# Kernel optimization log

Hardware: AMD Instinct MI355X
Metric: run time of the kernel (lower is better)

## Reference

```python
import jax, jax.numpy as jnp
import numpy as np

B, T, I, H = 128, 256, 512, 1024


def setup_inputs() -> dict:
    key = jax.random.key(0)
    ks = jax.random.split(key, 16)
    s_in = 1.0 / np.sqrt(I)
    s_h = 1.0 / np.sqrt(H)
    d = {
        "x": jax.random.normal(ks[0], (B, T, I), jnp.float32),
        "x_d": jax.random.normal(ks[1], (B, T, I), jnp.float32),
        "hidden": jnp.zeros((B, H), jnp.float32),
        "cell": jnp.zeros((B, H), jnp.float32),
    }
    for j, n in enumerate(["Wii", "Wif", "Wig", "Wio", "Wid", "Wro"]):
        d[n] = (jax.random.normal(ks[2 + j], (H, I), jnp.float32) * s_in)
    for j, n in enumerate(["Whi", "Whf", "Whg", "Who", "Whd"]):
        d[n] = (jax.random.normal(ks[8 + j], (H, H), jnp.float32) * s_h)
    for n in ["bi", "bf", "bg", "bo", "bd", "Wrb"]:
        d[n] = jnp.zeros((H,), jnp.float32)
    return d


def reference(x, x_d, hidden, cell,
              Wii, Whi, bi, Wif, Whf, bf, Wig, Whg, bg,
              Wio, Who, bo, Wid, Whd, bd, Wro, Wrb):
    # Precompute input-to-hidden contributions for all timesteps: (B,T,H)
    pi = jnp.einsum('bti,hi->bth', x, Wii) + bi
    pf = jnp.einsum('bti,hi->bth', x, Wif) + bf
    pg = jnp.einsum('bti,hi->bth', x, Wig) + bg
    po = jnp.einsum('bti,hi->bth', x, Wio) + bo
    pd = jnp.einsum('bti,hi->bth', x_d, Wid) + bd

    def step(carry, inp):
        h, c = carry
        pi_t, pf_t, pg_t, po_t, pd_t = inp  # each (B,H)
        i_t = jax.nn.sigmoid(pi_t + h @ Whi.T)
        f_t = jax.nn.sigmoid(pf_t + h @ Whf.T)
        g_t = jnp.tanh(pg_t + h @ Whg.T)
        o_t = jax.nn.sigmoid(po_t + h @ Who.T)
        d_t = jax.nn.sigmoid(pd_t + h @ Whd.T)
        c_new = f_t * c + i_t * g_t + d_t
        h_new = o_t * jnp.tanh(c_new)
        return (h_new, c_new), h_new

    xs = tuple(jnp.swapaxes(a, 0, 1) for a in (pi, pf, pg, po, pd))  # (T,B,H)
    (h_last, c_last), hs = jax.lax.scan(step, (hidden, cell), xs)
    hs = jnp.swapaxes(hs, 0, 1)  # (B,T,H)

    # Output projection per timestep (original reuses Who for the readout)
    y = jnp.tanh(jnp.einsum('bti,hi->bth', x, Wro)
                 + jnp.einsum('bth,gh->btg', hs, Who) + Wrb)
    return y, h_last, c_last
```

## Files before the change

### kernel.cpp

```cpp
#include <hip/hip_runtime.h>


using bf16x8 = __attribute__((ext_vector_type(8))) __bf16;
using f32x4  = __attribute__((ext_vector_type(4))) float;

#define MFMA16(a, b, c) __builtin_amdgcn_mfma_f32_16x16x32_bf16(a, b, c, 0, 0, 0)

static __device__ __forceinline__ float b2f(ushort u) {
  union { unsigned int i; float f; } v; v.i = ((unsigned int)u) << 16; return v.f;
}
static __device__ __forceinline__ ushort f2b(float f) {
  union { float f; unsigned int i; } v; v.f = f;
  unsigned int x = v.i;
  return (ushort)((x + 0x7fffu + ((x >> 16) & 1u)) >> 16);
}
static __device__ __forceinline__ float sigm(float x) {
  return 1.0f / (1.0f + __expf(-x));
}
static __device__ __forceinline__ float tanhfast(float x) {
  float e = __expf(2.0f * x);
  return 1.0f - 2.0f / (e + 1.0f);
}

__global__ __launch_bounds__(256) void cvt_kernel(const float* __restrict__ src,
                                                  ushort* __restrict__ dst, int n)
{
  int i = (blockIdx.x * 256 + threadIdx.x) * 4;
  if (i < n) {
    float4 v = *(const float4*)(src + i);
    ushort4 o;
    o.x = f2b(v.x); o.y = f2b(v.y); o.z = f2b(v.z); o.w = f2b(v.w);
    *(ushort4*)(dst + i) = o;
  }
}

static __device__ __forceinline__ void gemm_kloop(
    const ushort* __restrict__ A, int lda,
    const ushort* __restrict__ Bw, int ldb, int K,
    ushort* As, ushort* Bs, f32x4 (&acc)[4][4])
{
  const int tid = threadIdx.x;
  const int l = tid & 63, w = tid >> 6;
  const int wm = (w >> 1) * 64, wn = (w & 1) * 64;
  const int lr = l & 15, quad = l >> 4;
  bf16x8* Asv = (bf16x8*)As;
  bf16x8* Bsv = (bf16x8*)Bs;
  for (int k0 = 0; k0 < K; k0 += 32) {
    __syncthreads();
#pragma unroll
    for (int it = 0; it < 2; ++it) {
      int c = it * 256 + tid;
      int row = c >> 2, seg = c & 3;
      Asv[c] = *(const bf16x8*)(A  + row * lda + k0 + seg * 8);
      Bsv[c] = *(const bf16x8*)(Bw + row * ldb + k0 + seg * 8);
    }
    __syncthreads();
    bf16x8 af[4], bfr[4];
#pragma unroll
    for (int i = 0; i < 4; ++i) af[i]  = Asv[(wm + i * 16 + lr) * 4 + quad];
#pragma unroll
    for (int j = 0; j < 4; ++j) bfr[j] = Bsv[(wn + j * 16 + lr) * 4 + quad];
#pragma unroll
    for (int i = 0; i < 4; ++i)
#pragma unroll
      for (int j = 0; j < 4; ++j)
        acc[i][j] = MFMA16(af[i], bfr[j], acc[i][j]);
  }
}

__global__ __launch_bounds__(256) void gemm_pre(
    const ushort* __restrict__ xb, const ushort* __restrict__ xdb,
    const ushort* __restrict__ Wb,
    const float* __restrict__ bias5, ushort* __restrict__ P,
    int t0, int lc)
{
  __shared__ __align__(16) ushort As[4096], Bs[4096];
  const int m0 = blockIdx.x * 128;
  const int n0 = blockIdx.y * 128;
  const int g = n0 >> 10;
  const ushort* A = (g == 4) ? xdb : xb;
  const ushort* Bw = Wb + g * 524288 + (n0 & 1023) * 512;
  const int cm1 = (1 << lc) - 1;

  const int tid = threadIdx.x;
  const int l = tid & 63, w = tid >> 6;
  const int wm = (w >> 1) * 64, wn = (w & 1) * 64;
  const int lr = l & 15, quad = l >> 4;
  f32x4 acc[4][4] = {};
  bf16x8* Asv = (bf16x8*)As;
  bf16x8* Bsv = (bf16x8*)Bs;

  for (int k0 = 0; k0 < 512; k0 += 32) {
    __syncthreads();
#pragma unroll
    for (int it = 0; it < 2; ++it) {
      int c = it * 256 + tid;
      int row = c >> 2, seg = c & 3;
      int gr = m0 + row;
      int arow = ((gr >> lc) << 8) + t0 + (gr & cm1);
      Asv[c] = *(const bf16x8*)(A  + arow * 512 + k0 + seg * 8);
      Bsv[c] = *(const bf16x8*)(Bw + row  * 512 + k0 + seg * 8);
    }
    __syncthreads();
    bf16x8 af[4], bfr[4];
#pragma unroll
    for (int i = 0; i < 4; ++i) af[i]  = Asv[(wm + i * 16 + lr) * 4 + quad];
#pragma unroll
    for (int j = 0; j < 4; ++j) bfr[j] = Bsv[(wn + j * 16 + lr) * 4 + quad];
#pragma unroll
    for (int i = 0; i < 4; ++i)
#pragma unroll
      for (int j = 0; j < 4; ++j)
        acc[i][j] = MFMA16(af[i], bfr[j], acc[i][j]);
  }

#pragma unroll
  for (int i = 0; i < 4; ++i)
#pragma unroll
    for (int j = 0; j < 4; ++j) {
      int row = m0 + wm + i * 16 + quad * 4;
      int col = n0 + wn + j * 16 + lr;
      float bias = bias5[col];
#pragma unroll
      for (int r = 0; r < 4; ++r)
        P[(row + r) * 5120 + col] = f2b(acc[i][j][r] + bias);
    }
}

__global__ __launch_bounds__(256, 1) void lstm_chunk(
    const ushort* __restrict__ h0,
    float* __restrict__ cbuf, const ushort* __restrict__ Whb,
    const ushort* __restrict__ P, ushort* __restrict__ hs,
    unsigned int* __restrict__ flags, unsigned int* __restrict__ release,
    int t0, int nt, int lc)
{
  __shared__ __align__(16) ushort Bs0[32 * 64 * 8];
  __shared__ __align__(16) ushort Bs1[32 * 64 * 8];
  __shared__ float Pls[128 * 21];
  __shared__ float cs[128 * 5];

  const int tid = threadIdx.x;
  const int l = tid & 63, w = tid >> 6;
  const int lr = l & 15, quad = l >> 4;
  const int nb = blockIdx.x;

  {
    const ushort* wp = Whb + (((lr >> 2) << 10) + nb * 4 + (lr & 3)) * 1024 + quad * 8;
#pragma unroll
    for (int kk = 0; kk < 8; ++kk) {
      int k = w * 8 + kk;
      *(bf16x8*)(Bs0 + (k * 64 + l) * 8) = *(const bf16x8*)(wp + k * 32);
    }
  }
  {
    const ushort* wp = Whb + (4096 + nb * 4 + (lr & 3)) * 1024 + quad * 8;
#pragma unroll
    for (int kk = 0; kk < 8; ++kk) {
      int k = w * 8 + kk;
      bf16x8 v = {};
      if (lr < 4) v = *(const bf16x8*)(wp + k * 32);
      *(bf16x8*)(Bs1 + (k * 64 + l) * 8) = v;
    }
  }
  if (tid < 128) {
    float4 cv = *(const float4*)(cbuf + tid * 1024 + nb * 4);
    cs[tid * 5 + 0] = cv.x; cs[tid * 5 + 1] = cv.y;
    cs[tid * 5 + 2] = cv.z; cs[tid * 5 + 3] = cv.w;
  }
  __syncthreads();

  const bf16x8* B0v = (const bf16x8*)Bs0;
  const bf16x8* B1v = (const bf16x8*)Bs1;

  const int eb = tid >> 1;
  const int hp = (tid & 1) * 2;

  ushort2 q0, q1, q2, q3, q4;
  {
    const int prow = ((eb << lc) + 0) * 5120 + nb * 4 + hp;
    q0 = *(const ushort2*)(P + prow);
    q1 = *(const ushort2*)(P + prow + 1024);
    q2 = *(const ushort2*)(P + prow + 2048);
    q3 = *(const ushort2*)(P + prow + 3072);
    q4 = *(const ushort2*)(P + prow + 4096);
  }

  for (int tt = 0; tt < nt; ++tt) {
    const int t = t0 + tt;
    const ushort* base;
    int rs;
    if (t == 0) { base = h0;                 rs = 1024;   }
    else        { base = hs + (t - 1) * 1024; rs = 262144; }
    const ushort* a0p = base + (w * 32 + lr) * rs + quad * 8;
    const ushort* a1p = a0p + 16 * rs;

    f32x4 acc[2][2] = {};
#pragma unroll
    for (int k = 0; k < 32; ++k) {
      bf16x8 a0 = *(const bf16x8*)(a0p + k * 32);
      bf16x8 a1 = *(const bf16x8*)(a1p + k * 32);
      bf16x8 b0 = B0v[k * 64 + l];
      bf16x8 b1 = B1v[k * 64 + l];
      acc[0][0] = MFMA16(a0, b0, acc[0][0]);
      acc[1][0] = MFMA16(a1, b0, acc[1][0]);
      acc[0][1] = MFMA16(a0, b1, acc[0][1]);
      acc[1][1] = MFMA16(a1, b1, acc[1][1]);
    }

#pragma unroll
    for (int i = 0; i < 2; ++i) {
      int b = w * 32 + i * 16 + quad * 4;
#pragma unroll
      for (int r = 0; r < 4; ++r)
        Pls[(b + r) * 21 + lr] = acc[i][0][r];
      if (lr < 4) {
#pragma unroll
        for (int r = 0; r < 4; ++r)
          Pls[(b + r) * 21 + 16 + lr] = acc[i][1][r];
      }
    }
    __syncthreads();

    {
      const float* pr = Pls + eb * 21;
      float pi0 = b2f(q0.x) + pr[0 + hp],  pi1 = b2f(q0.y) + pr[1 + hp];
      float pf0 = b2f(q1.x) + pr[4 + hp],  pf1 = b2f(q1.y) + pr[5 + hp];
      float pg0 = b2f(q2.x) + pr[8 + hp],  pg1 = b2f(q2.y) + pr[9 + hp];
      float po0 = b2f(q3.x) + pr[12 + hp], po1 = b2f(q3.y) + pr[13 + hp];
      float pd0 = b2f(q4.x) + pr[16 + hp], pd1 = b2f(q4.y) + pr[17 + hp];
      float c0 = cs[eb * 5 + hp], c1 = cs[eb * 5 + hp + 1];
      float cn0 = sigm(pf0) * c0 + sigm(pi0) * tanhfast(pg0) + sigm(pd0);
      float cn1 = sigm(pf1) * c1 + sigm(pi1) * tanhfast(pg1) + sigm(pd1);
      cs[eb * 5 + hp] = cn0;
      cs[eb * 5 + hp + 1] = cn1;
      union { ushort2 s; unsigned int u; } hu;
      hu.s.x = f2b(sigm(po0) * tanhfast(cn0));
      hu.s.y = f2b(sigm(po1) * tanhfast(cn1));
      __hip_atomic_store(
          (unsigned int*)(hs + (eb * 256 + t) * 1024 + nb * 4 + hp),
          hu.u, __ATOMIC_RELAXED, __HIP_MEMORY_SCOPE_AGENT);
    }

    if (tt + 1 < nt) {
      const unsigned int g = (unsigned int)(t + 1);
      __syncthreads();
      if (tid == 0) {
        asm volatile("s_waitcnt vmcnt(0)" ::: "memory");
        __hip_atomic_store(flags + nb, g, __ATOMIC_RELAXED,
                           __HIP_MEMORY_SCOPE_AGENT);
      }
      {
        const int prow = ((eb << lc) + tt + 1) * 5120 + nb * 4 + hp;
        q0 = *(const ushort2*)(P + prow);
        q1 = *(const ushort2*)(P + prow + 1024);
        q2 = *(const ushort2*)(P + prow + 2048);
        q3 = *(const ushort2*)(P + prow + 3072);
        q4 = *(const ushort2*)(P + prow + 4096);
      }
      if (nb == 0 && tid < 64) {
        for (;;) {
          unsigned int f0 = __hip_atomic_load(flags + tid * 4 + 0,
                              __ATOMIC_RELAXED, __HIP_MEMORY_SCOPE_AGENT);
          unsigned int f1 = __hip_atomic_load(flags + tid * 4 + 1,
                              __ATOMIC_RELAXED, __HIP_MEMORY_SCOPE_AGENT);
          unsigned int f2 = __hip_atomic_load(flags + tid * 4 + 2,
                              __ATOMIC_RELAXED, __HIP_MEMORY_SCOPE_AGENT);
          unsigned int f3 = __hip_atomic_load(flags + tid * 4 + 3,
                              __ATOMIC_RELAXED, __HIP_MEMORY_SCOPE_AGENT);
          bool ok = (f0 >= g) & (f1 >= g) & (f2 >= g) & (f3 >= g);
          if (__all(ok)) break;
          __builtin_amdgcn_s_sleep(1);
        }
        if (tid == 0)
          __hip_atomic_store(release, g, __ATOMIC_RELAXED,
                             __HIP_MEMORY_SCOPE_AGENT);
      }
      while (__hip_atomic_load(release, __ATOMIC_RELAXED,
                               __HIP_MEMORY_SCOPE_AGENT) < g) {
        __builtin_amdgcn_s_sleep(1);
      }
      asm volatile("" ::: "memory");
    }
  }

  *(float2*)(cbuf + eb * 1024 + nb * 4 + hp) = *(float2*)(cs + eb * 5 + hp);
}

__global__ __launch_bounds__(64) void lstm_step(
    const ushort* __restrict__ h0, float* __restrict__ cbuf,
    const ushort* __restrict__ Whb, const ushort* __restrict__ P,
    ushort* __restrict__ hs, int t, int tloc, int lc)
{
  const int l = threadIdx.x;
  const int m0 = blockIdx.x * 32;
  const int hc = blockIdx.y * 16;
  const int lr = l & 15, quad = l >> 4;

  const ushort* base;
  int rs;
  if (t == 0) { base = h0;                 rs = 1024;   }
  else        { base = hs + (t - 1) * 1024; rs = 262144; }

  f32x4 acc[2][5] = {};
  const ushort* a0p = base + (m0 + lr) * rs + quad * 8;
  const ushort* a1p = a0p + 16 * rs;
  const ushort* wp = Whb + (hc + lr) * 1024 + quad * 8;

#pragma unroll 2
  for (int k0 = 0; k0 < 1024; k0 += 32) {
    bf16x8 a0 = *(const bf16x8*)(a0p + k0);
    bf16x8 a1 = *(const bf16x8*)(a1p + k0);
    bf16x8 b0 = *(const bf16x8*)(wp + k0);
    bf16x8 b1 = *(const bf16x8*)(wp + 1048576 + k0);
    bf16x8 b2 = *(const bf16x8*)(wp + 2097152 + k0);
    bf16x8 b3 = *(const bf16x8*)(wp + 3145728 + k0);
    bf16x8 b4 = *(const bf16x8*)(wp + 4194304 + k0);
    acc[0][0] = MFMA16(a0, b0, acc[0][0]);
    acc[1][0] = MFMA16(a1, b0, acc[1][0]);
    acc[0][1] = MFMA16(a0, b1, acc[0][1]);
    acc[1][1] = MFMA16(a1, b1, acc[1][1]);
    acc[0][2] = MFMA16(a0, b2, acc[0][2]);
    acc[1][2] = MFMA16(a1, b2, acc[1][2]);
    acc[0][3] = MFMA16(a0, b3, acc[0][3]);
    acc[1][3] = MFMA16(a1, b3, acc[1][3]);
    acc[0][4] = MFMA16(a0, b4, acc[0][4]);
    acc[1][4] = MFMA16(a1, b4, acc[1][4]);
  }

  const int h = hc + lr;
#pragma unroll
  for (int i = 0; i < 2; ++i) {
#pragma unroll
    for (int r = 0; r < 4; ++r) {
      int b = m0 + i * 16 + quad * 4 + r;
      int prow = ((b << lc) + tloc) * 5120;
      float pi = b2f(P[prow + h])          + acc[i][0][r];
      float pf = b2f(P[prow + 1024 + h])   + acc[i][1][r];
      float pg = b2f(P[prow + 2048 + h])   + acc[i][2][r];
      float po = b2f(P[prow + 3072 + h])   + acc[i][3][r];
      float pd = b2f(P[prow + 4096 + h])   + acc[i][4][r];
      float ig = sigm(pi), fg = sigm(pf), gg = tanhfast(pg);
      float og = sigm(po), dg = sigm(pd);
      float cold = cbuf[b * 1024 + h];
      float cnew = fg * cold + ig * gg + dg;
      cbuf[b * 1024 + h] = cnew;
      hs[(b * 256 + t) * 1024 + h] = f2b(og * tanhfast(cnew));
    }
  }
}

__global__ __launch_bounds__(256) void gemm_post(
    const ushort* __restrict__ xb, const ushort* __restrict__ hs,
    const ushort* __restrict__ Wrob, const ushort* __restrict__ Whob,
    const float* __restrict__ Wrb, float* __restrict__ y)
{
  __shared__ __align__(16) ushort As[4096], Bs[4096];
  const int m0 = blockIdx.x * 128;
  const int n0 = blockIdx.y * 128;
  f32x4 acc[4][4] = {};
  gemm_kloop(xb + m0 * 512,  512,  Wrob + n0 * 512,  512,  512,  As, Bs, acc);
  gemm_kloop(hs + m0 * 1024, 1024, Whob + n0 * 1024, 1024, 1024, As, Bs, acc);

  const int tid = threadIdx.x;
  const int l = tid & 63, w = tid >> 6;
  const int wm = (w >> 1) * 64, wn = (w & 1) * 64;
  const int lr = l & 15, quad = l >> 4;
#pragma unroll
  for (int i = 0; i < 4; ++i)
#pragma unroll
    for (int j = 0; j < 4; ++j) {
      int row = m0 + wm + i * 16 + quad * 4;
      int col = n0 + wn + j * 16 + lr;
      float bias = Wrb[col];
#pragma unroll
      for (int r = 0; r < 4; ++r)
        y[(row + r) * 1024 + col] = tanhfast(acc[i][j][r] + bias);
    }
}

__global__ __launch_bounds__(256) void finish_kernel(
    const ushort* __restrict__ hs, const float* __restrict__ cbuf,
    float* __restrict__ out_tail)
{
  int i = blockIdx.x * 256 + threadIdx.x;
  if (i < 131072) {
    int b = i >> 10, h = i & 1023;
    out_tail[i] = b2f(hs[(b * 256 + 255) * 1024 + h]);
    out_tail[131072 + i] = cbuf[i];
  }
}

extern "C" void kernel_launch(void* const* d_in, const int* in_sizes, int n_in,
                              void* d_out, int out_size, void* d_ws, size_t ws_size,
                              hipStream_t stream)
{
  const float* x   = (const float*)d_in[0];
  const float* xd  = (const float*)d_in[1];
  const float* hid = (const float*)d_in[2];
  const float* cel = (const float*)d_in[3];
  const float* Win[6] = {(const float*)d_in[4], (const float*)d_in[5],
                         (const float*)d_in[6], (const float*)d_in[7],
                         (const float*)d_in[8], (const float*)d_in[9]};
  const float* Whn[5] = {(const float*)d_in[10], (const float*)d_in[11],
                         (const float*)d_in[12], (const float*)d_in[13],
                         (const float*)d_in[14]};
  const float* bia[5] = {(const float*)d_in[15], (const float*)d_in[16],
                         (const float*)d_in[17], (const float*)d_in[18],
                         (const float*)d_in[19]};
  const float* Wrb = (const float*)d_in[20];
  float* y = (float*)d_out;

  char* ws = (char*)d_ws;
  ushort* xb    = (ushort*)(ws);
  ushort* xdb   = (ushort*)(ws + 33554432);
  ushort* Wb    = (ushort*)(ws + 67108864);
  ushort* Whb   = (ushort*)(ws + 73400320);
  ushort* hs    = (ushort*)(ws + 83886080);
  ushort* h0    = (ushort*)(ws + 150994944);
  float*  cbuf  = (float*) (ws + 151519232);
  float*  bias5 = (float*) (ws + 152043520);
  unsigned int* flags = (unsigned int*)(ws + 152064000);
  unsigned int* release = flags + 512;
  ushort* P     = (ushort*)(ws + 152068096);

  int chunk = 1;
  for (int c = 256; c >= 1; c >>= 1)
    if (152068096ull + (unsigned long long)c * 1310720ull <= (unsigned long long)ws_size) {
      chunk = c; break;
    }
  int lc = 31 - __builtin_clz((unsigned)chunk);

  cvt_kernel<<<16384, 256, 0, stream>>>(x,  xb,  16777216);
  cvt_kernel<<<16384, 256, 0, stream>>>(xd, xdb, 16777216);
  for (int i = 0; i < 6; ++i)
    cvt_kernel<<<512, 256, 0, stream>>>(Win[i], Wb + i * 524288, 524288);
  for (int i = 0; i < 5; ++i)
    cvt_kernel<<<1024, 256, 0, stream>>>(Whn[i], Whb + i * 1048576, 1048576);
  cvt_kernel<<<128, 256, 0, stream>>>(hid, h0, 131072);
  hipMemcpyAsync(cbuf, cel, 131072 * 4, hipMemcpyDeviceToDevice, stream);
  for (int i = 0; i < 5; ++i)
    hipMemcpyAsync(bias5 + i * 1024, bia[i], 4096, hipMemcpyDeviceToDevice, stream);
  hipMemsetAsync(flags, 0, 4096, stream);

  int t = 0;
  bool coop_ok = true;
  for (int c = 0; c < 256 / chunk; ++c) {
    gemm_pre<<<dim3(chunk, 40), 256, 0, stream>>>(xb, xdb, Wb, bias5, P,
                                                  c * chunk, lc);
    if (coop_ok) {
      int t0 = c * chunk;
      void* args[] = {&h0, &cbuf, &Whb, &P, &hs, &flags, &release,
                      &t0, &chunk, &lc};
      hipError_t e = hipLaunchCooperativeKernel((const void*)lstm_chunk,
                                                dim3(256), dim3(256),
                                                args, 0, stream);
      if (e == hipSuccess) {
        t += chunk;
        continue;
      }
      coop_ok = false;
    }
    for (int tt = 0; tt < chunk; ++tt, ++t)
      lstm_step<<<dim3(4, 64), 64, 0, stream>>>(h0, cbuf, Whb, P, hs,
                                                t, tt, lc);
  }
  gemm_post<<<dim3(256, 8), 256, 0, stream>>>(xb, hs, Wb + 5 * 524288,
                                              Whb + 3 * 1048576, Wrb, y);
  finish_kernel<<<512, 256, 0, stream>>>(hs, cbuf, y + 33554432);
}
```

Measured before the change: 3.988 ms.

## Fuse input projection into persistent LSTM kernel and use counter barrier

Moves the per-timestep input-to-hidden GEMM into the persistent cooperative LSTM kernel. Each block keeps its slice of the input weights in shared memory and computes the next step's pre-activations into a double-buffered LDS tile while waiting at the grid barrier. This removes the separate gemm_pre launches and the global P round trip. The flag-array barrier polled by block 0 is replaced by a single atomic counter whose last arriver sets the release word. The cost is more LDS per block and extra x reads on the serial path, which may lengthen each step if the barrier wait does not hide them.

```diff
diff --git a/kernel.cpp b/kernel.cpp
--- a/kernel.cpp
+++ b/kernel.cpp
@@ -71,8 +71,7 @@
 __global__ __launch_bounds__(256) void gemm_pre(
     const ushort* __restrict__ xb, const ushort* __restrict__ xdb,
     const ushort* __restrict__ Wb,
-    const float* __restrict__ bias5, ushort* __restrict__ P,
-    int t0, int lc)
+    const float* __restrict__ bias5, ushort* __restrict__ P, int t0)
 {
   __shared__ __align__(16) ushort As[4096], Bs[4096];
   const int m0 = blockIdx.x * 128;
@@ -80,7 +79,6 @@
   const int g = n0 >> 10;
   const ushort* A = (g == 4) ? xdb : xb;
   const ushort* Bw = Wb + g * 524288 + (n0 & 1023) * 512;
-  const int cm1 = (1 << lc) - 1;
 
   const int tid = threadIdx.x;
   const int l = tid & 63, w = tid >> 6;
@@ -97,7 +95,7 @@
       int c = it * 256 + tid;
       int row = c >> 2, seg = c & 3;
       int gr = m0 + row;
-      int arow = ((gr >> lc) << 8) + t0 + (gr & cm1);
+      int arow = gr * 256 + t0;
       Asv[c] = *(const bf16x8*)(A  + arow * 512 + k0 + seg * 8);
       Bsv[c] = *(const bf16x8*)(Bw + row  * 512 + k0 + seg * 8);
     }
@@ -127,22 +125,27 @@
     }
 }
 
-__global__ __launch_bounds__(256, 1) void lstm_chunk(
-    const ushort* __restrict__ h0,
-    float* __restrict__ cbuf, const ushort* __restrict__ Whb,
-    const ushort* __restrict__ P, ushort* __restrict__ hs,
-    unsigned int* __restrict__ flags, unsigned int* __restrict__ release,
-    int t0, int nt, int lc)
+__global__ __launch_bounds__(256, 1) void lstm_fused(
+    const ushort* __restrict__ h0, float* __restrict__ cbuf,
+    const ushort* __restrict__ Whb, const ushort* __restrict__ Wib,
+    const ushort* __restrict__ xb, const ushort* __restrict__ xdb,
+    const float* __restrict__ bias5, ushort* __restrict__ hs,
+    unsigned int* __restrict__ ctr, unsigned int* __restrict__ release,
+    int nt)
 {
   __shared__ __align__(16) ushort Bs0[32 * 64 * 8];
   __shared__ __align__(16) ushort Bs1[32 * 64 * 8];
-  __shared__ float Pls[128 * 21];
-  __shared__ float cs[128 * 5];
+  __shared__ __align__(16) ushort Wi0[16 * 64 * 8];
+  __shared__ __align__(16) ushort Wi1[16 * 64 * 8];
+  __shared__ float  Pls[128 * 21];
+  __shared__ ushort Pbuf[2][128 * 21];
+  __shared__ float  cs[128 * 5];
 
   const int tid = threadIdx.x;
   const int l = tid & 63, w = tid >> 6;
   const int lr = l & 15, quad = l >> 4;
   const int nb = blockIdx.x;
+  const unsigned int nblk = gridDim.x;
 
   {
     const ushort* wp = Whb + (((lr >> 2) << 10) + nb * 4 + (lr & 3)) * 1024 + quad * 8;
@@ -162,6 +165,26 @@
       *(bf16x8*)(Bs1 + (k * 64 + l) * 8) = v;
     }
   }
+  {
+    const ushort* wp = Wib + (lr >> 2) * 524288 + (nb * 4 + (lr & 3)) * 512 + quad * 8;
+#pragma unroll
+    for (int kk = 0; kk < 4; ++kk) {
+      int k = w * 4 + kk;
+      *(bf16x8*)(Wi0 + (k * 64 + l) * 8) = *(const bf16x8*)(wp + k * 32);
+    }
+  }
+  {
+    const ushort* wp = Wib + 4 * 524288 + (nb * 4 + (lr & 3)) * 512 + quad * 8;
+#pragma unroll
+    for (int kk = 0; kk < 4; ++kk) {
+      int k = w * 4 + kk;
+      bf16x8 v = {};
+      if (lr < 4) v = *(const bf16x8*)(wp + k * 32);
+      *(bf16x8*)(Wi1 + (k * 64 + l) * 8) = v;
+    }
+  }
+  const float b0l = bias5[((lr >> 2) << 10) + nb * 4 + (lr & 3)];
+  const float b1l = (lr < 4) ? bias5[4096 + nb * 4 + lr] : 0.0f;
   if (tid < 128) {
     float4 cv = *(const float4*)(cbuf + tid * 1024 + nb * 4);
     cs[tid * 5 + 0] = cv.x; cs[tid * 5 + 1] = cv.y;
@@ -171,25 +194,51 @@
 
   const bf16x8* B0v = (const bf16x8*)Bs0;
   const bf16x8* B1v = (const bf16x8*)Bs1;
+  const bf16x8* W0v = (const bf16x8*)Wi0;
+  const bf16x8* W1v = (const bf16x8*)Wi1;
 
   const int eb = tid >> 1;
   const int hp = (tid & 1) * 2;
 
-  ushort2 q0, q1, q2, q3, q4;
-  {
-    const int prow = ((eb << lc) + 0) * 5120 + nb * 4 + hp;
-    q0 = *(const ushort2*)(P + prow);
-    q1 = *(const ushort2*)(P + prow + 1024);
-    q2 = *(const ushort2*)(P + prow + 2048);
-    q3 = *(const ushort2*)(P + prow + 3072);
-    q4 = *(const ushort2*)(P + prow + 4096);
-  }
+  auto pregemm = [&](int t, int pb) {
+    const ushort* ax = xb  + (w * 32 + lr) * 131072 + t * 512 + quad * 8;
+    const ushort* ad = xdb + (w * 32 + lr) * 131072 + t * 512 + quad * 8;
+    f32x4 ap[2][2] = {};
+#pragma unroll
+    for (int k = 0; k < 16; ++k) {
+      bf16x8 x0 = *(const bf16x8*)(ax + k * 32);
+      bf16x8 x1 = *(const bf16x8*)(ax + 16 * 131072 + k * 32);
+      bf16x8 d0 = *(const bf16x8*)(ad + k * 32);
+      bf16x8 d1 = *(const bf16x8*)(ad + 16 * 131072 + k * 32);
+      bf16x8 w0 = W0v[k * 64 + l];
+      bf16x8 w1 = W1v[k * 64 + l];
+      ap[0][0] = MFMA16(x0, w0, ap[0][0]);
+      ap[1][0] = MFMA16(x1, w0, ap[1][0]);
+      ap[0][1] = MFMA16(d0, w1, ap[0][1]);
+      ap[1][1] = MFMA16(d1, w1, ap[1][1]);
+    }
+    ushort* dst = Pbuf[pb];
+#pragma unroll
+    for (int i = 0; i < 2; ++i) {
+      int b = w * 32 + i * 16 + quad * 4;
+#pragma unroll
+      for (int r = 0; r < 4; ++r)
+        dst[(b + r) * 21 + lr] = f2b(ap[i][0][r] + b0l);
+      if (lr < 4) {
+#pragma unroll
+        for (int r = 0; r < 4; ++r)
+          dst[(b + r) * 21 + 16 + lr] = f2b(ap[i][1][r] + b1l);
+      }
+    }
+  };
+
+  pregemm(0, 0);
 
   for (int tt = 0; tt < nt; ++tt) {
-    const int t = t0 + tt;
+    const int t = tt;
     const ushort* base;
     int rs;
-    if (t == 0) { base = h0;                 rs = 1024;   }
+    if (t == 0) { base = h0;                  rs = 1024;   }
     else        { base = hs + (t - 1) * 1024; rs = 262144; }
     const ushort* a0p = base + (w * 32 + lr) * rs + quad * 8;
     const ushort* a1p = a0p + 16 * rs;
@@ -222,12 +271,18 @@
     __syncthreads();
 
     {
-      const float* pr = Pls + eb * 21;
-      float pi0 = b2f(q0.x) + pr[0 + hp],  pi1 = b2f(q0.y) + pr[1 + hp];
-      float pf0 = b2f(q1.x) + pr[4 + hp],  pf1 = b2f(q1.y) + pr[5 + hp];
-      float pg0 = b2f(q2.x) + pr[8 + hp],  pg1 = b2f(q2.y) + pr[9 + hp];
-      float po0 = b2f(q3.x) + pr[12 + hp], po1 = b2f(q3.y) + pr[13 + hp];
-      float pd0 = b2f(q4.x) + pr[16 + hp], pd1 = b2f(q4.y) + pr[17 + hp];
+      const float*  pr = Pls + eb * 21;
+      const ushort* pp = Pbuf[tt & 1] + eb * 21;
+      float pi0 = b2f(pp[0 + hp])  + pr[0 + hp];
+      float pi1 = b2f(pp[1 + hp])  + pr[1 + hp];
+      float pf0 = b2f(pp[4 + hp])  + pr[4 + hp];
+      float pf1 = b2f(pp[5 + hp])  + pr[5 + hp];
+      float pg0 = b2f(pp[8 + hp])  + pr[8 + hp];
+      float pg1 = b2f(pp[9 + hp])  + pr[9 + hp];
+      float po0 = b2f(pp[12 + hp]) + pr[12 + hp];
+      float po1 = b2f(pp[13 + hp]) + pr[13 + hp];
+      float pd0 = b2f(pp[16 + hp]) + pr[16 + hp];
+      float pd1 = b2f(pp[17 + hp]) + pr[17 + hp];
       float c0 = cs[eb * 5 + hp], c1 = cs[eb * 5 + hp + 1];
       float cn0 = sigm(pf0) * c0 + sigm(pi0) * tanhfast(pg0) + sigm(pd0);
       float cn1 = sigm(pf1) * c1 + sigm(pi1) * tanhfast(pg1) + sigm(pd1);
@@ -246,35 +301,13 @@
       __syncthreads();
       if (tid == 0) {
         asm volatile("s_waitcnt vmcnt(0)" ::: "memory");
-        __hip_atomic_store(flags + nb, g, __ATOMIC_RELAXED,
-                           __HIP_MEMORY_SCOPE_AGENT);
-      }
-      {
-        const int prow = ((eb << lc) + tt + 1) * 5120 + nb * 4 + hp;
-        q0 = *(const ushort2*)(P + prow);
-        q1 = *(const ushort2*)(P + prow + 1024);
-        q2 = *(const ushort2*)(P + prow + 2048);
-        q3 = *(const ushort2*)(P + prow + 3072);
-        q4 = *(const ushort2*)(P + prow + 4096);
-      }
-      if (nb == 0 && tid < 64) {
-        for (;;) {
-          unsigned int f0 = __hip_atomic_load(flags + tid * 4 + 0,
-                              __ATOMIC_RELAXED, __HIP_MEMORY_SCOPE_AGENT);
-          unsigned int f1 = __hip_atomic_load(flags + tid * 4 + 1,
-                              __ATOMIC_RELAXED, __HIP_MEMORY_SCOPE_AGENT);
-          unsigned int f2 = __hip_atomic_load(flags + tid * 4 + 2,
-                              __ATOMIC_RELAXED, __HIP_MEMORY_SCOPE_AGENT);
-          unsigned int f3 = __hip_atomic_load(flags + tid * 4 + 3,
-                              __ATOMIC_RELAXED, __HIP_MEMORY_SCOPE_AGENT);
-          bool ok = (f0 >= g) & (f1 >= g) & (f2 >= g) & (f3 >= g);
-          if (__all(ok)) break;
-          __builtin_amdgcn_s_sleep(1);
-        }
-        if (tid == 0)
+        unsigned int old = __hip_atomic_fetch_add(ctr, 1u, __ATOMIC_RELAXED,
+                                                  __HIP_MEMORY_SCOPE_AGENT);
+        if (old == g * nblk - 1u)
           __hip_atomic_store(release, g, __ATOMIC_RELAXED,
                              __HIP_MEMORY_SCOPE_AGENT);
       }
+      pregemm(tt + 1, (tt + 1) & 1);
       while (__hip_atomic_load(release, __ATOMIC_RELAXED,
                                __HIP_MEMORY_SCOPE_AGENT) < g) {
         __builtin_amdgcn_s_sleep(1);
@@ -289,7 +322,7 @@
 __global__ __launch_bounds__(64) void lstm_step(
     const ushort* __restrict__ h0, float* __restrict__ cbuf,
     const ushort* __restrict__ Whb, const ushort* __restrict__ P,
-    ushort* __restrict__ hs, int t, int tloc, int lc)
+    ushort* __restrict__ hs, int t)
 {
   const int l = threadIdx.x;
   const int m0 = blockIdx.x * 32;
@@ -298,7 +331,7 @@
 
   const ushort* base;
   int rs;
-  if (t == 0) { base = h0;                 rs = 1024;   }
+  if (t == 0) { base = h0;                  rs = 1024;   }
   else        { base = hs + (t - 1) * 1024; rs = 262144; }
 
   f32x4 acc[2][5] = {};
@@ -333,7 +366,7 @@
 #pragma unroll
     for (int r = 0; r < 4; ++r) {
       int b = m0 + i * 16 + quad * 4 + r;
-      int prow = ((b << lc) + tloc) * 5120;
+      int prow = b * 5120;
       float pi = b2f(P[prow + h])          + acc[i][0][r];
       float pf = b2f(P[prow + 1024 + h])   + acc[i][1][r];
       float pg = b2f(P[prow + 2048 + h])   + acc[i][2][r];
@@ -420,15 +453,9 @@
   float*  cbuf  = (float*) (ws + 151519232);
   float*  bias5 = (float*) (ws + 152043520);
   unsigned int* flags = (unsigned int*)(ws + 152064000);
-  unsigned int* release = flags + 512;
+  unsigned int* ctr     = flags;
+  unsigned int* release = flags + 128;
   ushort* P     = (ushort*)(ws + 152068096);
-
-  int chunk = 1;
-  for (int c = 256; c >= 1; c >>= 1)
-    if (152068096ull + (unsigned long long)c * 1310720ull <= (unsigned long long)ws_size) {
-      chunk = c; break;
-    }
-  int lc = 31 - __builtin_clz((unsigned)chunk);
 
   cvt_kernel<<<16384, 256, 0, stream>>>(x,  xb,  16777216);
   cvt_kernel<<<16384, 256, 0, stream>>>(xd, xdb, 16777216);
@@ -442,28 +469,19 @@
     hipMemcpyAsync(bias5 + i * 1024, bia[i], 4096, hipMemcpyDeviceToDevice, stream);
   hipMemsetAsync(flags, 0, 4096, stream);
 
-  int t = 0;
-  bool coop_ok = true;
-  for (int c = 0; c < 256 / chunk; ++c) {
-    gemm_pre<<<dim3(chunk, 40), 256, 0, stream>>>(xb, xdb, Wb, bias5, P,
-                                                  c * chunk, lc);
-    if (coop_ok) {
-      int t0 = c * chunk;
-      void* args[] = {&h0, &cbuf, &Whb, &P, &hs, &flags, &release,
-                      &t0, &chunk, &lc};
-      hipError_t e = hipLaunchCooperativeKernel((const void*)lstm_chunk,
-                                                dim3(256), dim3(256),
-                                                args, 0, stream);
-      if (e == hipSuccess) {
-        t += chunk;
-        continue;
-      }
-      coop_ok = false;
-    }
-    for (int tt = 0; tt < chunk; ++tt, ++t)
-      lstm_step<<<dim3(4, 64), 64, 0, stream>>>(h0, cbuf, Whb, P, hs,
-                                                t, tt, lc);
-  }
+  int nt = 256;
+  void* args[] = {&h0, &cbuf, &Whb, &Wb, &xb, &xdb, &bias5, &hs,
+                  &ctr, &release, &nt};
+  hipError_t e = hipLaunchCooperativeKernel((const void*)lstm_fused,
+                                            dim3(256), dim3(256),
+                                            args, 0, stream);
+  if (e != hipSuccess) {
+    for (int t = 0; t < 256; ++t) {
+      gemm_pre<<<dim3(1, 40), 256, 0, stream>>>(xb, xdb, Wb, bias5, P, t);
+      lstm_step<<<dim3(4, 64), 64, 0, stream>>>(h0, cbuf, Whb, P, hs, t);
+    }
+  }
+
   gemm_post<<<dim3(256, 8), 256, 0, stream>>>(xb, hs, Wb + 5 * 524288,
                                               Whb + 3 * 1048576, Wrb, y);
   finish_kernel<<<512, 256, 0, stream>>>(hs, cbuf, y + 33554432);
```

New measurement: 4.699 ms. +17.8%, slower.
